# Kernel tuning notes

Measured on AMD Instinct MI355X. Metric: run time of the kernel, lower is better.

The kernel has to match this reference:

```python
import jax, jax.numpy as jnp
import numpy as np

PRE_NMS_TOPK = 6000
POST_NMS_TOPK = 1000
NMS_THRESH = 0.7
MIN_SIZE = 16.0
N = 1_000_000
H, W = 800, 1333


def setup_inputs() -> dict:
    key = jax.random.key(0)
    ki, kx, ky, kw, kh, kd, kl = jax.random.split(key, 7)
    image = jax.random.normal(ki, (1, H, W, 3), jnp.float32)
    # realistic anchors: centers uniform over image, sizes in [8, 228)
    cx = jax.random.uniform(kx, (N,), jnp.float32) * W
    cy = jax.random.uniform(ky, (N,), jnp.float32) * H
    aw = jax.random.uniform(kw, (N,), jnp.float32) * 220.0 + 8.0
    ah = jax.random.uniform(kh, (N,), jnp.float32) * 220.0 + 8.0
    anchors = jnp.stack([cx - 0.5 * aw, cy - 0.5 * ah, cx + 0.5 * aw, cy + 0.5 * ah], axis=1)
    bbox_deltas = jax.random.normal(kd, (N, 4), jnp.float32) * 0.1
    logits = jax.random.normal(kl, (N, 1), jnp.float32)
    return {"image": image, "anchors": anchors, "bbox_deltas": bbox_deltas, "logits": logits}


def _iou_matrix(boxes):
    # boxes: [K,4] as (x1,y1,x2,y2); IoU is symmetric in axis labeling,
    # matching tf.image.non_max_suppression's overlap math.
    x1, y1, x2, y2 = boxes[:, 0], boxes[:, 1], boxes[:, 2], boxes[:, 3]
    area = (x2 - x1) * (y2 - y1)
    ix1 = jnp.maximum(x1[:, None], x1[None, :])
    iy1 = jnp.maximum(y1[:, None], y1[None, :])
    ix2 = jnp.minimum(x2[:, None], x2[None, :])
    iy2 = jnp.minimum(y2[:, None], y2[None, :])
    inter = jnp.maximum(ix2 - ix1, 0.0) * jnp.maximum(iy2 - iy1, 0.0)
    union = area[:, None] + area[None, :] - inter
    return jnp.where(union > 0.0, inter / union, 0.0)


def _sequential_nms(iou, valid, thresh):
    # iou: [K,K]; boxes are already sorted by descending score.
    K = iou.shape[0]
    idx = jnp.arange(K)

    def step(keep, inp):
        i, row = inp
        ki = keep[i]
        suppress = ki & (row > thresh) & (idx > i)
        return keep & ~suppress, ki

    _, kept = jax.lax.scan(step, valid, (idx, iou))
    return kept  # [K] bool, in sorted order


def reference(image, anchors, bbox_deltas, logits):
    height = jnp.float32(image.shape[1])
    width = jnp.float32(image.shape[2])

    # --- box decode ---
    wa = anchors[:, 2] - anchors[:, 0]
    ha = anchors[:, 3] - anchors[:, 1]
    xa = anchors[:, 0] + 0.5 * wa
    ya = anchors[:, 1] + 0.5 * ha
    x = bbox_deltas[:, 0] * wa + xa
    y = bbox_deltas[:, 1] * ha + ya
    w = jnp.exp(bbox_deltas[:, 2]) * wa
    h = jnp.exp(bbox_deltas[:, 3]) * ha
    x1 = jnp.clip(x - 0.5 * w, 0.0, width - 1.0)
    y1 = jnp.clip(y - 0.5 * h, 0.0, height - 1.0)
    x2 = jnp.clip(x + 0.5 * w, 0.0, width - 1.0)
    y2 = jnp.clip(y + 0.5 * h, 0.0, height - 1.0)
    proposals = jnp.stack([x1, y1, x2, y2], axis=1)  # [N,4]

    # --- min-size filter (mask instead of dynamic gather) ---
    valid = ((x2 - x1) >= MIN_SIZE) & ((y2 - y1) >= MIN_SIZE)
    scores = jnp.where(valid, jax.nn.sigmoid(logits[:, 0]), -jnp.inf)

    # --- pre-NMS top-k ---
    top_scores, top_idx = jax.lax.top_k(scores, PRE_NMS_TOPK)
    top_boxes = proposals[top_idx]              # [K,4]
    top_valid = top_scores > -jnp.inf

    # --- NMS ---
    iou = _iou_matrix(top_boxes)
    kept = _sequential_nms(iou, top_valid, NMS_THRESH)

    # --- pack kept boxes (in score order) into fixed [POST,4], zero-padded ---
    rank = jnp.cumsum(kept.astype(jnp.int32)) - 1
    slot = jnp.where(kept, rank, POST_NMS_TOPK)  # invalid -> dropped
    out = jnp.zeros((POST_NMS_TOPK, 4), top_boxes.dtype)
    out = out.at[slot].set(top_boxes, mode="drop")
    return out
```

## Files before the change

kernel.cpp:

```cpp
#include <hip/hip_runtime.h>
#include <stdint.h>
#include <math.h>

#define N_ANCH   1000000
#define N4       (N_ANCH / 4)
#define NBLK256  ((N4 + 255) / 256)
#define PRE_K    6000
#define POST_K   1000
#define WORDS    94
#define ROWS     6016
#define W_IMG    1333.0f
#define H_IMG    800.0f

#define HB       128
#define NBIN     16384
#define NS       8192
#define RBLK     128

#define OLDK     16

#define OFF_KEYS   0x000000u
#define OFF_CTRL   0x410000u
#define OFF_CAND   0x410100u
#define OFF_BOXES  0x421000u
#define OFF_VALID  0x439000u
#define OFF_MASK   0x440000u
#define OFF_PART   OFF_MASK

__device__ __forceinline__ float ref_exp(float v) {
  return (float)exp((double)v);
}

__device__ __forceinline__ void decode_box(float ax, float ay, float az, float aw,
                                           float dx, float dy, float dz, float dw,
                                           float& x1, float& y1, float& x2, float& y2,
                                           bool& valid) {
  float wa = __fsub_rn(az, ax);
  float ha = __fsub_rn(aw, ay);
  float xa = __fadd_rn(ax, __fmul_rn(0.5f, wa));
  float ya = __fadd_rn(ay, __fmul_rn(0.5f, ha));
  float x  = __fadd_rn(__fmul_rn(dx, wa), xa);
  float y  = __fadd_rn(__fmul_rn(dy, ha), ya);
  float w  = __fmul_rn(ref_exp(dz), wa);
  float h  = __fmul_rn(ref_exp(dw), ha);
  float hw = __fmul_rn(0.5f, w);
  float hh = __fmul_rn(0.5f, h);
  x1 = fminf(fmaxf(__fsub_rn(x, hw), 0.0f), W_IMG - 1.0f);
  y1 = fminf(fmaxf(__fsub_rn(y, hh), 0.0f), H_IMG - 1.0f);
  x2 = fminf(fmaxf(__fadd_rn(x, hw), 0.0f), W_IMG - 1.0f);
  y2 = fminf(fmaxf(__fadd_rn(y, hh), 0.0f), H_IMG - 1.0f);
  valid = (__fsub_rn(x2, x1) >= 16.0f) && (__fsub_rn(y2, y1) >= 16.0f);
}

__device__ __forceinline__ uint64_t bcast64(uint64_t v, int lane) {
  uint32_t lo = (uint32_t)__builtin_amdgcn_readlane((int)(uint32_t)v, lane);
  uint32_t hi = (uint32_t)__builtin_amdgcn_readlane((int)(uint32_t)(v >> 32), lane);
  return ((uint64_t)hi << 32) | lo;
}

__device__ __forceinline__ uint64_t shflxor64(uint64_t v, int m) {
  uint32_t lo = (uint32_t)__shfl_xor((int)(uint32_t)v, m, 64);
  uint32_t hi = (uint32_t)__shfl_xor((int)(uint32_t)(v >> 32), m, 64);
  return ((uint64_t)hi << 32) | lo;
}

__global__ void __launch_bounds__(1024) k_score(const float4* __restrict__ anchors,
                                                const float4* __restrict__ deltas,
                                                const float*  __restrict__ logits,
                                                uint32_t* __restrict__ keys,
                                                uint32_t* __restrict__ part1) {
  __shared__ uint32_t lh[NBIN];
  int tid = threadIdx.x, lane = tid & 63;
  for (int b = tid; b < NBIN; b += 1024) lh[b] = 0u;
  __syncthreads();
  for (int i = blockIdx.x * 1024 + tid; i < N_ANCH; i += HB * 1024) {
    float4 a = anchors[i];
    float4 d = deltas[i];
    float wa = a.z - a.x, ha = a.w - a.y;
    float xa = a.x + 0.5f * wa, ya = a.y + 0.5f * ha;
    float x = d.x * wa + xa, y = d.y * ha + ya;
    float w = __expf(d.z) * wa, h = __expf(d.w) * ha;
    float fx1 = fminf(fmaxf(x - 0.5f * w, 0.0f), W_IMG - 1.0f);
    float fx2 = fminf(fmaxf(x + 0.5f * w, 0.0f), W_IMG - 1.0f);
    float fy1 = fminf(fmaxf(y - 0.5f * h, 0.0f), H_IMG - 1.0f);
    float fy2 = fminf(fmaxf(y + 0.5f * h, 0.0f), H_IMG - 1.0f);
    float X = fx2 - fx1, Y = fy2 - fy1;
    bool valid = (X >= 16.0f) && (Y >= 16.0f);
    if (fabsf(X - 16.0f) < 0.02f || fabsf(Y - 16.0f) < 0.02f) {
      float ex1, ey1, ex2, ey2; bool vv;
      decode_box(a.x, a.y, a.z, a.w, d.x, d.y, d.z, d.w, ex1, ey1, ex2, ey2, vv);
      valid = vv;
    }
    uint32_t u = __float_as_uint(logits[i]);
    uint32_t o = (u & 0x80000000u) ? ~u : (u | 0x80000000u);
    uint32_t kd = valid ? ~o : 0xFFFFFFFFu;
    keys[i] = kd;
    uint64_t invb = __ballot(!valid);
    if (valid) {
      atomicAdd(&lh[kd >> 18], 1u);
    } else if ((invb & ((1ull << lane) - 1ull)) == 0ull) {
      atomicAdd(&lh[NBIN - 1], (uint32_t)__popcll((unsigned long long)invb));
    }
  }
  __syncthreads();
  uint32_t* row = part1 + (size_t)blockIdx.x * (NBIN / 2);
  #pragma unroll
  for (int j = 0; j < 8; j++) {
    uint32_t lo = lh[16 * tid + 2 * j];
    uint32_t hi = lh[16 * tid + 2 * j + 1];
    row[8 * tid + j] = (lo & 0xFFFFu) | (hi << 16);
  }
}

__global__ void __launch_bounds__(1024) k_cut14(const uint32_t* __restrict__ part1,
                                                uint32_t* __restrict__ ctrl) {
  __shared__ uint32_t part[1024];
  int t = threadIdx.x;
  uint32_t acc[16];
  #pragma unroll
  for (int j = 0; j < 16; j++) acc[j] = 0u;
  for (int b = 0; b < HB; b++) {
    const uint32_t* row = part1 + (size_t)b * (NBIN / 2) + 8 * t;
    #pragma unroll
    for (int j = 0; j < 8; j++) {
      uint32_t w = row[j];
      acc[2 * j]     += w & 0xFFFFu;
      acc[2 * j + 1] += w >> 16;
    }
  }
  uint32_t tot = 0;
  #pragma unroll
  for (int j = 0; j < 16; j++) tot += acc[j];
  part[t] = tot;
  __syncthreads();
  uint32_t inc = tot;
  for (int off = 1; off < 1024; off <<= 1) {
    uint32_t u = (t >= off) ? part[t - off] : 0u;
    __syncthreads();
    inc += u;
    part[t] = inc;
    __syncthreads();
  }
  uint32_t ex = inc - tot;
  if (ex < PRE_K && inc >= PRE_K) {
    uint32_t run = ex;
    for (int j = 0; j < 16; j++) {
      if (run + acc[j] >= PRE_K) { ctrl[1] = (uint32_t)(16 * t + j); break; }
      run += acc[j];
    }
  }
  if (t == 1023 && inc < PRE_K) ctrl[1] = NBIN - 1;
}

__global__ void __launch_bounds__(256) k_compact(const uint4* __restrict__ keys4,
                                                 const float* __restrict__ logits,
                                                 uint32_t* ctrl,
                                                 uint64_t* __restrict__ cand) {
  __shared__ uint32_t wcnt[4];
  __shared__ uint32_t bbase_s;
  int tid = threadIdx.x, lane = tid & 63, wv = tid >> 6;
  uint32_t T = ctrl[1];
  int i4 = blockIdx.x * 256 + tid;
  uint4 kk = make_uint4(~0u, ~0u, ~0u, ~0u);
  if (i4 < N4) kk = keys4[i4];
  uint32_t ks[4] = { kk.x, kk.y, kk.z, kk.w };
  bool pass[4]; uint64_t m[4];
  uint32_t tot = 0;
  #pragma unroll
  for (int e = 0; e < 4; e++) {
    pass[e] = (i4 < N4) && ((ks[e] >> 18) <= T);
    m[e] = __ballot(pass[e]);
    tot += (uint32_t)__popcll((unsigned long long)m[e]);
  }
  if (lane == 0) wcnt[wv] = tot;
  __syncthreads();
  if (tid == 0) {
    uint32_t bt = wcnt[0] + wcnt[1] + wcnt[2] + wcnt[3];
    bbase_s = bt ? atomicAdd(&ctrl[0], bt) : 0u;
  }
  __syncthreads();
  uint32_t wb = bbase_s;
  for (int w2 = 0; w2 < wv; w2++) wb += wcnt[w2];
  uint64_t lmask = (1ull << lane) - 1ull;
  #pragma unroll
  for (int e = 0; e < 4; e++) {
    if (pass[e]) {
      int i = 4 * i4 + e;
      uint32_t skey;
      if (ks[e] == 0xFFFFFFFFu) {
        skey = 0xFF800000u;
      } else {
        double xd = (double)logits[i];
        float s = (float)(1.0 / (1.0 + exp(-xd)));
        skey = 0x7FFFFFFFu & ~__float_as_uint(s);
      }
      uint32_t p = wb + (uint32_t)__popcll((unsigned long long)(m[e] & lmask));
      if (p < NS) cand[p] = ((uint64_t)skey << 20) | (uint32_t)i;
    }
    wb += (uint32_t)__popcll((unsigned long long)m[e]);
  }
}

__global__ void __launch_bounds__(256) k_rank(
    const uint32_t* __restrict__ ctrl,
    const uint64_t* __restrict__ cand,
    const float4* __restrict__ anchors,
    const float4* __restrict__ deltas,
    float4* __restrict__ boxes,
    uint32_t* __restrict__ valid) {
  __shared__ uint32_t part[4][64];
  int tid = threadIdx.x;
  int wv = tid >> 6, lane = tid & 63;
  int i = blockIdx.x * 64 + lane;
  uint32_t M = ctrl[0]; if (M > NS) M = NS;
  uint64_t myk = (i < (int)M) ? cand[i] : ~0ull;
  uint32_t cnt = 0;
  const int QUART = NS / 4;
  int jbase = wv * QUART;
  for (int s = 0; s < QUART / 64; s++) {
    int j = jbase + s * 64 + lane;
    uint64_t c = (j < (int)M) ? cand[j] : ~0ull;
    #pragma unroll
    for (int s2 = 0; s2 < 64; s2++) {
      uint64_t kb = bcast64(c, s2);
      cnt += (kb < myk) ? 1u : 0u;
    }
  }
  part[wv][lane] = cnt;
  __syncthreads();
  if (wv != 0) return;
  uint32_t rank = part[0][lane] + part[1][lane] + part[2][lane] + part[3][lane];
  if (i < (int)M && rank < PRE_K) {
    uint32_t skey = (uint32_t)(myk >> 20);
    uint32_t idx  = (uint32_t)(myk & 0xFFFFFu);
    if (skey >= 0xFF800000u) {
      boxes[rank] = make_float4(0.f, 0.f, 0.f, 0.f);
      valid[rank] = 0u;
    } else {
      float4 a = anchors[idx];
      float4 d = deltas[idx];
      float x1, y1, x2, y2; bool vv;
      decode_box(a.x, a.y, a.z, a.w, d.x, d.y, d.z, d.w, x1, y1, x2, y2, vv);
      boxes[rank] = make_float4(x1, y1, x2, y2);
      valid[rank] = 1u;
    }
  }
  if ((i >= (int)M || i >= PRE_K) && i < ROWS) {
    boxes[i] = make_float4(0.f, 0.f, 0.f, 0.f);
    valid[i] = 0u;
  }
}

__global__ void __launch_bounds__(64) k_iou(const float4* __restrict__ boxes,
                                            uint64_t* __restrict__ mask) {
  int by = blockIdx.y, bx = blockIdx.x;
  if (bx < by) return;
  __shared__ float4 cb[64];
  int t = threadIdx.x;
  cb[t] = boxes[bx * 64 + t];
  __syncthreads();
  int i = by * 64 + t;
  float4 b = boxes[i];
  float ax1 = b.x, ay1 = b.y, ax2 = b.z, ay2 = b.w;
  float areaA = __fmul_rn(__fsub_rn(ax2, ax1), __fsub_rn(ay2, ay1));
  uint64_t bits = 0;
  for (int c = 0; c < 64; c++) {
    float4 o = cb[c];
    float areaB = __fmul_rn(__fsub_rn(o.z, o.x), __fsub_rn(o.w, o.y));
    float ix1 = fmaxf(ax1, o.x), iy1 = fmaxf(ay1, o.y);
    float ix2 = fminf(ax2, o.z), iy2 = fminf(ay2, o.w);
    float iw = fmaxf(__fsub_rn(ix2, ix1), 0.0f);
    float ih = fmaxf(__fsub_rn(iy2, iy1), 0.0f);
    float inter = __fmul_rn(iw, ih);
    float uni = __fsub_rn(__fadd_rn(areaA, areaB), inter);
    bool sup = (uni > 0.0f) && (__fdiv_rn(inter, uni) > 0.7f);
    bits |= ((uint64_t)sup) << c;
  }
  mask[(size_t)i * WORDS + bx] = bits;
}

__global__ void __launch_bounds__(64, 1) k_nms(const uint64_t* __restrict__ mask,
                                               const float4* __restrict__ boxes,
                                               const uint32_t* __restrict__ valid,
                                               float* __restrict__ out) {
  __shared__ uint32_t list[1088];
  int lane = threadIdx.x;
  uint64_t lmask = (1ull << lane) - 1ull;
  int cnt = 0;
  uint64_t colv = mask[(size_t)lane * WORDS + 0];
  uint32_t vf = valid[lane];
  uint64_t cur = 0;
  for (int g = 0; g < WORDS; g++) {
    int base = g * 64;
    bool haveNext = (g + 1 < WORDS);
    uint64_t newv = 0, colv_n = 0, oldv[OLDK];
    uint32_t vf_n = 0, om = 0;
    if (haveNext) {
      newv   = mask[(size_t)(base + lane) * WORDS + (g + 1)];
      colv_n = mask[(size_t)(base + 64 + lane) * WORDS + (g + 1)];
      vf_n   = valid[base + 64 + lane];
      #pragma unroll
      for (int k = 0; k < OLDK; k++) {
        int t = 64 * k + lane;
        uint32_t row = (t < cnt) ? list[t] : 0u;
        om |= (t < cnt) ? (1u << k) : 0u;
        oldv[k] = mask[(size_t)row * WORDS + (g + 1)];
      }
    }
    uint64_t vmask = __ballot(vf != 0u);
    uint64_t alive = vmask & ~cur;
    uint64_t kept = 0;
    #pragma unroll
    for (int r = 0; r < 64; r++) {
      uint64_t mr = bcast64(colv, r);
      uint64_t take = (alive >> r) & 1ull;
      kept |= take << r;
      alive &= ~(take ? mr : 0ull);
    }
    uint32_t below = (uint32_t)__popcll((unsigned long long)(kept & lmask));
    if ((kept >> lane) & 1ull) {
      uint32_t pos = (uint32_t)cnt + below;
      if (pos < 1088u) list[pos] = (uint32_t)(base + lane);
    }
    cnt += (int)__popcll((unsigned long long)kept);
    if (cnt >= POST_K || !haveNext) break;
    asm volatile("" : "+v"(newv),
                      "+v"(oldv[0]),  "+v"(oldv[1]),  "+v"(oldv[2]),  "+v"(oldv[3]),
                      "+v"(oldv[4]),  "+v"(oldv[5]),  "+v"(oldv[6]),  "+v"(oldv[7]),
                      "+v"(oldv[8]),  "+v"(oldv[9]),  "+v"(oldv[10]), "+v"(oldv[11]),
                      "+v"(oldv[12]), "+v"(oldv[13]), "+v"(oldv[14]), "+v"(oldv[15]));
    uint64_t acc = ((kept >> lane) & 1ull) ? newv : 0ull;
    #pragma unroll
    for (int k = 0; k < OLDK; k++)
      acc |= oldv[k] & (0ull - (uint64_t)((om >> k) & 1u));
    #pragma unroll
    for (int off = 1; off < 64; off <<= 1)
      acc |= shflxor64(acc, off);
    cur = bcast64(acc, 0);
    colv = colv_n; vf = vf_n;
  }
  __syncthreads();
  float4* outv = (float4*)out;
  for (int k = lane; k < POST_K; k += 64)
    outv[k] = (k < cnt) ? boxes[list[k]] : make_float4(0.f, 0.f, 0.f, 0.f);
}

extern "C" void kernel_launch(void* const* d_in, const int* in_sizes, int n_in,
                              void* d_out, int out_size, void* d_ws, size_t ws_size,
                              hipStream_t stream) {
  const float4* anchors = (const float4*)d_in[1];
  const float4* deltas  = (const float4*)d_in[2];
  const float*  logits  = (const float*)d_in[3];
  char* w = (char*)d_ws;
  uint32_t* keys  = (uint32_t*)(w + OFF_KEYS);
  uint32_t* part1 = (uint32_t*)(w + OFF_PART);
  uint32_t* ctrl  = (uint32_t*)(w + OFF_CTRL);
  uint64_t* cand  = (uint64_t*)(w + OFF_CAND);
  float4*   boxes = (float4*)(w + OFF_BOXES);
  uint32_t* valid = (uint32_t*)(w + OFF_VALID);
  uint64_t* mask  = (uint64_t*)(w + OFF_MASK);
  float*    out   = (float*)d_out;

  hipMemsetAsync(w + OFF_CTRL, 0, 256, stream);

  k_score<<<HB, 1024, 0, stream>>>(anchors, deltas, logits, keys, part1);
  k_cut14<<<1, 1024, 0, stream>>>(part1, ctrl);
  k_compact<<<NBLK256, 256, 0, stream>>>((const uint4*)keys, logits, ctrl, cand);
  k_rank<<<RBLK, 256, 0, stream>>>(ctrl, cand, anchors, deltas, boxes, valid);
  k_iou<<<dim3(WORDS, WORDS), 64, 0, stream>>>(boxes, mask);
  k_nms<<<1, 64, 0, stream>>>(mask, boxes, valid, out);
}
```

Baseline: 264.8 us.

## Merge per-block histograms with global atomics and use coarser 13-bit bins

The score kernel now merges its shared-memory histogram straight into one global histogram with atomics, replacing the per-block partial rows the cut kernel had to sum serially. Bins shrink from 16384 to 8192 (key shift 19) and the grid grows from 128 to 245 blocks to fill more CUs. The cut kernel then reads only 8 bins per thread. Coarser bins can let more candidates past the threshold into compaction and ranking, and the global atomics add contention on the hot bins.

```diff
diff --git a/kernel.cpp b/kernel.cpp
--- a/kernel.cpp
+++ b/kernel.cpp
@@ -12,20 +12,21 @@
 #define W_IMG    1333.0f
 #define H_IMG    800.0f
 
-#define HB       128
-#define NBIN     16384
+#define HB       245
+#define NBIN     8192
+#define KSHIFT   19
 #define NS       8192
 #define RBLK     128
 
 #define OLDK     16
 
 #define OFF_KEYS   0x000000u
-#define OFF_CTRL   0x410000u
-#define OFF_CAND   0x410100u
-#define OFF_BOXES  0x421000u
-#define OFF_VALID  0x439000u
+#define OFF_CTRL   0x400000u
+#define OFF_HIST   0x400100u
+#define OFF_CAND   0x410000u
+#define OFF_BOXES  0x420000u
+#define OFF_VALID  0x438000u
 #define OFF_MASK   0x440000u
-#define OFF_PART   OFF_MASK
 
 __device__ __forceinline__ float ref_exp(float v) {
   return (float)exp((double)v);
@@ -68,7 +69,7 @@
                                                 const float4* __restrict__ deltas,
                                                 const float*  __restrict__ logits,
                                                 uint32_t* __restrict__ keys,
-                                                uint32_t* __restrict__ part1) {
+                                                uint32_t* __restrict__ hist) {
   __shared__ uint32_t lh[NBIN];
   int tid = threadIdx.x, lane = tid & 63;
   for (int b = tid; b < NBIN; b += 1024) lh[b] = 0u;
@@ -97,40 +98,28 @@
     keys[i] = kd;
     uint64_t invb = __ballot(!valid);
     if (valid) {
-      atomicAdd(&lh[kd >> 18], 1u);
+      atomicAdd(&lh[kd >> KSHIFT], 1u);
     } else if ((invb & ((1ull << lane) - 1ull)) == 0ull) {
       atomicAdd(&lh[NBIN - 1], (uint32_t)__popcll((unsigned long long)invb));
     }
   }
   __syncthreads();
-  uint32_t* row = part1 + (size_t)blockIdx.x * (NBIN / 2);
-  #pragma unroll
-  for (int j = 0; j < 8; j++) {
-    uint32_t lo = lh[16 * tid + 2 * j];
-    uint32_t hi = lh[16 * tid + 2 * j + 1];
-    row[8 * tid + j] = (lo & 0xFFFFu) | (hi << 16);
-  }
-}
-
-__global__ void __launch_bounds__(1024) k_cut14(const uint32_t* __restrict__ part1,
+  for (int b = tid; b < NBIN; b += 1024) {
+    uint32_t cv = lh[b];
+    if (cv) atomicAdd(&hist[b], cv);
+  }
+}
+
+__global__ void __launch_bounds__(1024) k_cut13(const uint32_t* __restrict__ hist,
                                                 uint32_t* __restrict__ ctrl) {
   __shared__ uint32_t part[1024];
   int t = threadIdx.x;
-  uint32_t acc[16];
-  #pragma unroll
-  for (int j = 0; j < 16; j++) acc[j] = 0u;
-  for (int b = 0; b < HB; b++) {
-    const uint32_t* row = part1 + (size_t)b * (NBIN / 2) + 8 * t;
-    #pragma unroll
-    for (int j = 0; j < 8; j++) {
-      uint32_t w = row[j];
-      acc[2 * j]     += w & 0xFFFFu;
-      acc[2 * j + 1] += w >> 16;
-    }
-  }
+  const uint4* h4 = (const uint4*)hist;
+  uint4 q0 = h4[2 * t], q1 = h4[2 * t + 1];
+  uint32_t b[8] = { q0.x, q0.y, q0.z, q0.w, q1.x, q1.y, q1.z, q1.w };
   uint32_t tot = 0;
   #pragma unroll
-  for (int j = 0; j < 16; j++) tot += acc[j];
+  for (int j = 0; j < 8; j++) tot += b[j];
   part[t] = tot;
   __syncthreads();
   uint32_t inc = tot;
@@ -144,9 +133,9 @@
   uint32_t ex = inc - tot;
   if (ex < PRE_K && inc >= PRE_K) {
     uint32_t run = ex;
-    for (int j = 0; j < 16; j++) {
-      if (run + acc[j] >= PRE_K) { ctrl[1] = (uint32_t)(16 * t + j); break; }
-      run += acc[j];
+    for (int j = 0; j < 8; j++) {
+      if (run + b[j] >= PRE_K) { ctrl[1] = (uint32_t)(8 * t + j); break; }
+      run += b[j];
     }
   }
   if (t == 1023 && inc < PRE_K) ctrl[1] = NBIN - 1;
@@ -168,7 +157,7 @@
   uint32_t tot = 0;
   #pragma unroll
   for (int e = 0; e < 4; e++) {
-    pass[e] = (i4 < N4) && ((ks[e] >> 18) <= T);
+    pass[e] = (i4 < N4) && ((ks[e] >> KSHIFT) <= T);
     m[e] = __ballot(pass[e]);
     tot += (uint32_t)__popcll((unsigned long long)m[e]);
   }
@@ -353,18 +342,18 @@
   const float*  logits  = (const float*)d_in[3];
   char* w = (char*)d_ws;
   uint32_t* keys  = (uint32_t*)(w + OFF_KEYS);
-  uint32_t* part1 = (uint32_t*)(w + OFF_PART);
   uint32_t* ctrl  = (uint32_t*)(w + OFF_CTRL);
+  uint32_t* hist  = (uint32_t*)(w + OFF_HIST);
   uint64_t* cand  = (uint64_t*)(w + OFF_CAND);
   float4*   boxes = (float4*)(w + OFF_BOXES);
   uint32_t* valid = (uint32_t*)(w + OFF_VALID);
   uint64_t* mask  = (uint64_t*)(w + OFF_MASK);
   float*    out   = (float*)d_out;
 
-  hipMemsetAsync(w + OFF_CTRL, 0, 256, stream);
-
-  k_score<<<HB, 1024, 0, stream>>>(anchors, deltas, logits, keys, part1);
-  k_cut14<<<1, 1024, 0, stream>>>(part1, ctrl);
+  hipMemsetAsync(w + OFF_CTRL, 0, 0x8100, stream);
+
+  k_score<<<HB, 1024, 0, stream>>>(anchors, deltas, logits, keys, hist);
+  k_cut13<<<1, 1024, 0, stream>>>(hist, ctrl);
   k_compact<<<NBLK256, 256, 0, stream>>>((const uint4*)keys, logits, ctrl, cand);
   k_rank<<<RBLK, 256, 0, stream>>>(ctrl, cand, anchors, deltas, boxes, valid);
   k_iou<<<dim3(WORDS, WORDS), 64, 0, stream>>>(boxes, mask);
```

Result: faster. 225.2 us (-15.0%).
